# Kernel tuning notes

Measured on AMD Instinct MI355X. Metric: run time of the kernel, lower is better.

## Reference

```python
import jax, jax.numpy as jnp
import numpy as np

N_HEAD = 8
D_MODEL = 512
D_HEAD = D_MODEL // N_HEAD
D_HIDDEN = 2048
LN_EPS = 1e-5


def setup_inputs() -> dict:
    key = jax.random.key(0)
    ks = jax.random.split(key, 13)
    s = 0.02
    return {
        "spatial_features": jax.random.normal(ks[0], (4096, 64, D_MODEL), dtype=jnp.float32),
        "Wk": jax.random.normal(ks[1], (D_MODEL, D_MODEL), dtype=jnp.float32) * s,
        "bk": jnp.zeros((D_MODEL,), dtype=jnp.float32),
        "Wv": jax.random.normal(ks[2], (D_MODEL, D_MODEL), dtype=jnp.float32) * s,
        "bv": jnp.zeros((D_MODEL,), dtype=jnp.float32),
        "score_w": jax.random.normal(ks[3], (N_HEAD, D_HEAD), dtype=jnp.float32) * s,
        "score_b": jnp.zeros((N_HEAD,), dtype=jnp.float32),
        "W1": jax.random.normal(ks[4], (D_MODEL, D_HIDDEN), dtype=jnp.float32) * s,
        "b1": jnp.zeros((D_HIDDEN,), dtype=jnp.float32),
        "W2": jax.random.normal(ks[5], (D_HIDDEN, D_MODEL), dtype=jnp.float32) * s,
        "b2": jnp.zeros((D_MODEL,), dtype=jnp.float32),
        "ln_g": jnp.ones((D_MODEL,), dtype=jnp.float32),
        "ln_b": jnp.zeros((D_MODEL,), dtype=jnp.float32),
    }


def reference(spatial_features, Wk, bk, Wv, bv, score_w, score_b,
              W1, b1, W2, b2, ln_g, ln_b):
    B, N, _ = spatial_features.shape
    # k, v projections -> [B, N, H, Dh]
    k = (spatial_features @ Wk + bk).reshape(B, N, N_HEAD, D_HEAD)
    v = (spatial_features @ Wv + bv).reshape(B, N, N_HEAD, D_HEAD)
    # per-head score: Linear(d_head -> 1) batched over heads
    score = jnp.einsum('bnhd,hd->bnh', k, score_w) + score_b  # [B, N, H]
    attn = jax.nn.softmax(score, axis=1)                       # softmax over N
    # weighted sum pooling over N, then concat heads -> [B, d_model]
    feature = jnp.einsum('bnh,bnhd->bhd', attn, v).reshape(B, D_MODEL)
    # FFN with residual + layernorm (dropout = eval identity)
    h = jax.nn.gelu(feature @ W1 + b1, approximate=False)
    y = h @ W2 + b2 + feature
    mu = jnp.mean(y, axis=-1, keepdims=True)
    var = jnp.mean((y - mu) ** 2, axis=-1, keepdims=True)
    out = (y - mu) * jax.lax.rsqrt(var + LN_EPS) * ln_g + ln_b
    return out
```

## Files before the change

kernel.cpp:

```cpp
#include <hip/hip_runtime.h>
#include <hip/hip_bf16.h>

#define N_HEAD 8
#define D_MODEL 512
#define D_HEAD 64
#define D_HIDDEN 2048
#define NTOK 64
#define BATCH 4096

typedef __attribute__((ext_vector_type(4))) float f32x4;
typedef __attribute__((ext_vector_type(8))) short short8;
typedef __attribute__((ext_vector_type(8))) unsigned short u16x8;
typedef __attribute__((ext_vector_type(4))) unsigned short u16x4;

__device__ __forceinline__ float bf2f(unsigned short u) {
    return __uint_as_float(((unsigned int)u) << 16);
}
__device__ __forceinline__ unsigned short f2bf(float f) {
    unsigned int b = __float_as_uint(f);
    b += 0x7fffu + ((b >> 16) & 1u);
    return (unsigned short)(b >> 16);
}
__device__ __forceinline__ float wave_sum(float v) {
    v += __shfl_xor(v, 32); v += __shfl_xor(v, 16); v += __shfl_xor(v, 8);
    v += __shfl_xor(v, 4);  v += __shfl_xor(v, 2);  v += __shfl_xor(v, 1);
    return v;
}
__device__ __forceinline__ void gload_lds16(const void* g, void* l) {
    __builtin_amdgcn_global_load_lds(
        (const __attribute__((address_space(1))) unsigned int*)g,
        (__attribute__((address_space(3))) unsigned int*)l, 16, 0, 0);
}

__global__ __launch_bounds__(256) void prep_all(
    const float* __restrict__ Wk, const float* __restrict__ score_w,
    const float* __restrict__ Wv, const float* __restrict__ W1,
    const float* __restrict__ W2,
    unsigned short* __restrict__ uT,
    unsigned short* __restrict__ WvT, unsigned short* __restrict__ W1T,
    unsigned short* __restrict__ W2T) {
    int m = blockIdx.y;
    if (m == 3) {
        int idx = blockIdx.x * 256 + threadIdx.x;
        if (idx < 16 * 512) {
            int h = idx & 15, c = idx >> 4;
            float s = 0.f;
            if (h < 8) {
                #pragma unroll 8
                for (int d = 0; d < D_HEAD; ++d)
                    s += Wk[c * D_MODEL + h * D_HEAD + d] * score_w[h * D_HEAD + d];
            }
            uT[h * D_MODEL + c] = f2bf(s);
        }
        return;
    }
    const float* in; unsigned short* out; int K, N, tX, tiles;
    if (m == 0)      { in = Wv; out = WvT; K = 512;  N = 512;  tX = 16; tiles = 256;  }
    else if (m == 1) { in = W1; out = W1T; K = 512;  N = 2048; tX = 64; tiles = 1024; }
    else             { in = W2; out = W2T; K = 2048; N = 512;  tX = 16; tiles = 1024; }
    int t = blockIdx.x;
    if (t >= tiles) return;
    int n0 = (t % tX) * 32, k0 = (t / tX) * 32;
    __shared__ float tile[32][33];
    int tx = threadIdx.x & 31, ty = threadIdx.x >> 5;
    #pragma unroll
    for (int i = ty; i < 32; i += 8)
        tile[i][tx] = in[(size_t)(k0 + i) * N + n0 + tx];
    __syncthreads();
    #pragma unroll
    for (int i = ty; i < 32; i += 8)
        out[(size_t)(n0 + i) * K + k0 + tx] = f2bf(tile[tx][i]);
}

__global__ void score_pool_v15(
    const float* __restrict__ x, const unsigned short* __restrict__ uT,
    unsigned short* __restrict__ pooled) {
    __shared__ unsigned short xl[16 * D_MODEL];
    __shared__ unsigned short ul[8 * D_MODEL];
    __shared__ float el[16 * 8];
    __shared__ float zacc[8];

    const int tid = threadIdx.x;
    const int l = tid & 63, w = tid >> 6;
    const int hg = l >> 4, lr = l & 15;

    {
        int r = tid >> 6;
        int c8 = (tid & 63) * 8;
        u16x8 v = *(const u16x8*)(uT + r * D_MODEL + c8);
        *(u16x8*)&ul[r * D_MODEL + (c8 ^ (r << 3))] = v;
    }

    const int tr4 = tid >> 7;
    const int col4 = (tid & 127) * 4;

    const int c2 = (tid & 255) * 2;
    const int hh = tid >> 8;

    const int b0 = blockIdx.x * 4;

    float4 preA[4], preB[4];
    {
        const float4* p0 = (const float4*)(x + (size_t)b0 * (NTOK * D_MODEL));
        const float4* p1 = (const float4*)(x + (size_t)b0 * (NTOK * D_MODEL) +
                                           16 * D_MODEL);
        #pragma unroll
        for (int j = 0; j < 4; ++j) preA[j] = p0[j * 512 + tid];
        #pragma unroll
        for (int j = 0; j < 4; ++j) preB[j] = p1[j * 512 + tid];
    }

    f32x4 acc0 = {0.f, 0.f, 0.f, 0.f};
    f32x4 acc1 = {0.f, 0.f, 0.f, 0.f};

    int qq = 0;

#define QSTEP(BUF)                                                             \
    {                                                                          \
        const int q = qq & 3;                                                  \
        if (q == 0 && tid < 8) zacc[tid] = 0.f;                                \
        _Pragma("unroll")                                                      \
        for (int j = 0; j < 4; ++j) {                                          \
            int row = j * 4 + tr4;                                             \
            float4 a = BUF[j];                                                 \
            u16x4 ov = {f2bf(a.x), f2bf(a.y), f2bf(a.z), f2bf(a.w)};           \
            *(u16x4*)&xl[row * D_MODEL + (col4 ^ ((row & 7) << 3))] = ov;      \
        }                                                                      \
        if (qq < 14) {                                                         \
            const int nb = b0 + ((qq + 2) >> 2), nq = (qq + 2) & 3;            \
            const float4* p = (const float4*)(x +                              \
                (size_t)nb * (NTOK * D_MODEL) + nq * 16 * D_MODEL);            \
            _Pragma("unroll")                                                  \
            for (int j = 0; j < 4; ++j) BUF[j] = p[j * 512 + tid];             \
        }                                                                      \
        asm volatile("s_waitcnt lgkmcnt(0)" ::: "memory");                     \
        __builtin_amdgcn_s_barrier();                                   \
        if (w == (qq & 7)) {                                                   \
            f32x4 sacc = {0.f, 0.f, 0.f, 0.f};                                 \
            const int rbase = lr * D_MODEL;                                    \
            const int rsw = (lr & 7) << 3;                                     \
            _Pragma("unroll")                                                  \
            for (int ks = 0; ks < 16; ++ks) {                                  \
                int off = ks * 32 + hg * 8;                                    \
                short8 uf;                                                     \
                if (lr < 8) uf = *(const short8*)&ul[lr * D_MODEL +            \
                                                     (off ^ (lr << 3))];       \
                else        uf = (short8){0, 0, 0, 0, 0, 0, 0, 0};             \
                short8 xf = *(const short8*)&xl[rbase + (off ^ rsw)];          \
                sacc = __builtin_amdgcn_mfma_f32_16x16x32_bf16(uf, xf, sacc,   \
                                                               0, 0, 0);       \
            }                                                                  \
            f32x4 ev;                                                          \
            float zsum[4];                                                     \
            _Pragma("unroll")                                                  \
            for (int j = 0; j < 4; ++j) {                                      \
                float e = __expf(sacc[j]);                                     \
                ev[j] = e;                                                     \
                e += __shfl_xor(e, 1); e += __shfl_xor(e, 2);                  \
                e += __shfl_xor(e, 4); e += __shfl_xor(e, 8);                  \
                zsum[j] = e;                                                   \
            }                                                                  \
            if (hg < 2) {                                                      \
                *(f32x4*)&el[lr * 8 + hg * 4] = ev;                            \
                if (lr == 0) {                                                 \
                    f32x4 z = *(const f32x4*)&zacc[hg * 4];                    \
                    z[0] += zsum[0]; z[1] += zsum[1];                          \
                    z[2] += zsum[2]; z[3] += zsum[3];                          \
                    *(f32x4*)&zacc[hg * 4] = z;                                \
                }                                                              \
            }                                                                  \
        }                                                                      \
        asm volatile("s_waitcnt lgkmcnt(0)" ::: "memory");                     \
        __builtin_amdgcn_s_barrier();                                   \
        _Pragma("unroll 4")                                                    \
        for (int t = 0; t < 16; ++t) {                                         \
            unsigned int xw = *(const unsigned int*)&xl[t * D_MODEL +          \
                                                  (c2 ^ ((t & 7) << 3))];      \
            f32x4 e4 = *(const f32x4*)&el[t * 8 + hh * 4];                     \
            float xa = __uint_as_float(xw << 16);                              \
            float xb = __uint_as_float(xw & 0xffff0000u);                      \
            acc0 += e4 * xa;                                                   \
            acc1 += e4 * xb;                                                   \
        }                                                                      \
        if (q == 3) {                                                          \
            f32x4 z = *(const f32x4*)&zacc[hh * 4];                            \
            unsigned short* pb = pooled +                                      \
                (size_t)(b0 + (qq >> 2)) * (N_HEAD * D_MODEL);                 \
            _Pragma("unroll")                                                  \
            for (int hq = 0; hq < 4; ++hq) {                                   \
                float rzq = 1.f / z[hq];                                       \
                unsigned int pk = (unsigned int)f2bf(acc0[hq] * rzq) |         \
                                  ((unsigned int)f2bf(acc1[hq] * rzq) << 16);  \
                *(unsigned int*)(pb + (hh * 4 + hq) * D_MODEL + c2) = pk;      \
            }                                                                  \
            acc0 = (f32x4){0.f, 0.f, 0.f, 0.f};                                \
            acc1 = (f32x4){0.f, 0.f, 0.f, 0.f};                                \
        }                                                                      \
        asm volatile("s_waitcnt lgkmcnt(0)" ::: "memory");                     \
        __builtin_amdgcn_s_barrier();                                   \
        ++qq;                                                                  \
    }

    #pragma unroll 1
    for (int it = 0; it < 8; ++it) {
        QSTEP(preA)
        QSTEP(preB)
    }
#undef QSTEP
}

template <int BM, int BN, int MODE>
__global__ __launch_bounds__(256) void gemm_mf(
    const unsigned short* __restrict__ A, int lda,
    const unsigned short* __restrict__ BT,
    const float* __restrict__ bias,
    void* __restrict__ Cout, int ldc,
    const unsigned short* __restrict__ res, int K) {
    __shared__ unsigned short Al[BM * 64];
    __shared__ unsigned short Bl[BN * 64];
    int m0 = blockIdx.x * BM;
    int n0;
    const unsigned short* Ap = A;
    const unsigned short* Bp;
    const float* bp;
    if (MODE == 0) {
        int h = blockIdx.y;
        Ap = A + (size_t)h * 512;
        Bp = BT + (size_t)h * 64 * K;
        bp = bias + h * 64;
        n0 = h * 64;
    } else {
        n0 = blockIdx.y * BN;
        Bp = BT + (size_t)n0 * K;
        bp = bias + n0;
    }
    int tid = threadIdx.x, l = tid & 63, w = tid >> 6;
    int lr = l & 15, lq = l >> 4;
    int wm = w >> 1, wn = w & 1;
    constexpr int MR = BM / 32, NR = BN / 32;
    constexpr int AI = BM / 8, BI = BN / 8;

    f32x4 acc[MR][NR];
    #pragma unroll
    for (int mi = 0; mi < MR; ++mi)
        #pragma unroll
        for (int nj = 0; nj < NR; ++nj) acc[mi][nj] = (f32x4){0.f, 0.f, 0.f, 0.f};

    int srow = l >> 3;
    int scol = ((l & 7) ^ ((l >> 3) & 7)) << 3;

    for (int k0 = 0; k0 < K; k0 += 64) {
        #pragma unroll
        for (int j = 0; j < AI / 4; ++j) {
            int ji = w * (AI / 4) + j;
            const unsigned short* src = Ap + (size_t)(m0 + ji * 8 + srow) * lda + k0 + scol;
            gload_lds16(src, &Al[ji * 512]);
        }
        #pragma unroll
        for (int j = 0; j < BI / 4; ++j) {
            int ji = w * (BI / 4) + j;
            const unsigned short* src = Bp + (size_t)(ji * 8 + srow) * K + k0 + scol;
            gload_lds16(src, &Bl[ji * 512]);
        }
        __syncthreads();
        #pragma unroll
        for (int kk = 0; kk < 64; kk += 32) {
            int sw = (kk + lq * 8) ^ ((l & 7) << 3);
            short8 af[MR], bf[NR];
            #pragma unroll
            for (int mi = 0; mi < MR; ++mi)
                af[mi] = *(const short8*)&Al[(wm * (BM / 2) + mi * 16 + lr) * 64 + sw];
            #pragma unroll
            for (int nj = 0; nj < NR; ++nj)
                bf[nj] = *(const short8*)&Bl[(wn * (BN / 2) + nj * 16 + lr) * 64 + sw];
            #pragma unroll
            for (int mi = 0; mi < MR; ++mi)
                #pragma unroll
                for (int nj = 0; nj < NR; ++nj)
                    acc[mi][nj] = __builtin_amdgcn_mfma_f32_16x16x32_bf16(
                        af[mi], bf[nj], acc[mi][nj], 0, 0, 0);
        }
        __syncthreads();
    }

    #pragma unroll
    for (int mi = 0; mi < MR; ++mi) {
        #pragma unroll
        for (int nj = 0; nj < NR; ++nj) {
            #pragma unroll
            for (int j = 0; j < 4; ++j) {
                int row = m0 + wm * (BM / 2) + mi * 16 + lq * 4 + j;
                int nl = wn * (BN / 2) + nj * 16 + lr;
                int col = n0 + nl;
                float v = acc[mi][nj][j] + bp[nl];
                if (MODE == 1) {
                    v = 0.5f * v * (1.0f + erff(v * 0.70710678118654752f));
                }
                if (MODE == 2) {
                    v += bf2f(res[(size_t)row * 512 + col]);
                    ((float*)Cout)[(size_t)row * ldc + col] = v;
                } else {
                    ((unsigned short*)Cout)[(size_t)row * ldc + col] = f2bf(v);
                }
            }
        }
    }
}

__global__ __launch_bounds__(256) void ln_kernel(
    float* __restrict__ y, const float* __restrict__ g, const float* __restrict__ bta) {
    int row = blockIdx.x * 4 + (threadIdx.x >> 6);
    int l = threadIdx.x & 63;
    float* yp = y + (size_t)row * D_MODEL;
    float4 v0 = *(const float4*)(yp + l * 8);
    float4 v1 = *(const float4*)(yp + l * 8 + 4);
    float vv[8] = {v0.x, v0.y, v0.z, v0.w, v1.x, v1.y, v1.z, v1.w};
    float s = 0.f;
    #pragma unroll
    for (int i = 0; i < 8; ++i) s += vv[i];
    s = wave_sum(s);
    float mean = s * (1.f / 512.f);
    float q = 0.f;
    #pragma unroll
    for (int i = 0; i < 8; ++i) { float d = vv[i] - mean; q += d * d; }
    q = wave_sum(q);
    float rstd = rsqrtf(q * (1.f / 512.f) + 1e-5f);
    float4 g0 = *(const float4*)(g + l * 8);
    float4 g1 = *(const float4*)(g + l * 8 + 4);
    float4 b0 = *(const float4*)(bta + l * 8);
    float4 b1 = *(const float4*)(bta + l * 8 + 4);
    float gv[8] = {g0.x, g0.y, g0.z, g0.w, g1.x, g1.y, g1.z, g1.w};
    float bv[8] = {b0.x, b0.y, b0.z, b0.w, b1.x, b1.y, b1.z, b1.w};
    float ov[8];
    #pragma unroll
    for (int i = 0; i < 8; ++i) ov[i] = (vv[i] - mean) * rstd * gv[i] + bv[i];
    float4 o0 = {ov[0], ov[1], ov[2], ov[3]};
    float4 o1 = {ov[4], ov[5], ov[6], ov[7]};
    *(float4*)(yp + l * 8) = o0;
    *(float4*)(yp + l * 8 + 4) = o1;
}

extern "C" void kernel_launch(void* const* d_in, const int* in_sizes, int n_in,
                              void* d_out, int out_size, void* d_ws, size_t ws_size,
                              hipStream_t stream) {
    const float* x       = (const float*)d_in[0];
    const float* Wk      = (const float*)d_in[1];
    const float* Wv      = (const float*)d_in[3];
    const float* bv      = (const float*)d_in[4];
    const float* score_w = (const float*)d_in[5];
    const float* W1      = (const float*)d_in[7];
    const float* b1      = (const float*)d_in[8];
    const float* W2      = (const float*)d_in[9];
    const float* b2      = (const float*)d_in[10];
    const float* ln_g    = (const float*)d_in[11];
    const float* ln_b    = (const float*)d_in[12];
    float* out = (float*)d_out;

    char* ws = (char*)d_ws;
    size_t off = 0;
    auto alloc = [&](size_t sz) {
        void* p = ws + off;
        off = (off + sz + 1023) & ~(size_t)1023;
        return p;
    };
    unsigned short* uT  = (unsigned short*)alloc((size_t)16 * D_MODEL * 2);
    unsigned short* WvT = (unsigned short*)alloc((size_t)512 * 512 * 2);
    unsigned short* W1T = (unsigned short*)alloc((size_t)2048 * 512 * 2);
    unsigned short* W2T = (unsigned short*)alloc((size_t)512 * 2048 * 2);
    unsigned short* pooled = (unsigned short*)alloc((size_t)BATCH * N_HEAD * D_MODEL * 2);
    unsigned short* feat   = (unsigned short*)alloc((size_t)BATCH * D_MODEL * 2);
    unsigned short* Hbuf   = (unsigned short*)alloc((size_t)BATCH * D_HIDDEN * 2);

    prep_all<<<dim3(1024, 4), dim3(256), 0, stream>>>(
        Wk, score_w, Wv, W1, W2, uT, WvT, W1T, W2T);
    score_pool_v15<<<dim3(1024), dim3(512), 0, stream>>>(x, uT, pooled);
    gemm_mf<128, 64, 0><<<dim3(32, 8), dim3(256), 0, stream>>>(
        pooled, N_HEAD * D_MODEL, WvT, bv, (void*)feat, D_MODEL,
        (const unsigned short*)nullptr, 512);
    gemm_mf<128, 128, 1><<<dim3(32, 16), dim3(256), 0, stream>>>(
        feat, D_MODEL, W1T, b1, (void*)Hbuf, D_HIDDEN,
        (const unsigned short*)nullptr, 512);
    gemm_mf<64, 128, 2><<<dim3(64, 4), dim3(256), 0, stream>>>(
        Hbuf, D_HIDDEN, W2T, b2, (void*)out, D_MODEL, feat, 2048);
    ln_kernel<<<dim3(1024), dim3(256), 0, stream>>>(out, ln_g, ln_b);
}
```

Measured before the change: 209.9 us.

## Software-pipeline score/pool kernel across three LDS stages with one barrier per step

Restructures the score+pool loop into a three-stage pipeline. Each step stores tile qq to LDS, computes scores for tile qq-1 and does the weighted pooling for tile qq-2, using a triple-buffered x tile and double-buffered exp/normaliser arrays. This cuts the barriers per step from two to one and lets the single-wave MFMA score work overlap with the pooling FMAs. It costs more LDS (three 16KB x buffers) and adds two extra drain iterations, which may lower occupancy.

```diff
diff --git a/kernel.cpp b/kernel.cpp
--- a/kernel.cpp
+++ b/kernel.cpp
@@ -72,13 +72,13 @@
         out[(size_t)(n0 + i) * K + k0 + tx] = f2bf(tile[tx][i]);
 }
 
-__global__ void score_pool_v15(
+__global__ __launch_bounds__(512) void score_pool_v16(
     const float* __restrict__ x, const unsigned short* __restrict__ uT,
     unsigned short* __restrict__ pooled) {
-    __shared__ unsigned short xl[16 * D_MODEL];
+    __shared__ unsigned short xl[3][16 * D_MODEL];
     __shared__ unsigned short ul[8 * D_MODEL];
-    __shared__ float el[16 * 8];
-    __shared__ float zacc[8];
+    __shared__ float el[2][16 * 8];
+    __shared__ float zacc[2][8];
 
     const int tid = threadIdx.x;
     const int l = tid & 63, w = tid >> 6;
@@ -117,25 +117,29 @@
 
 #define QSTEP(BUF)                                                             \
     {                                                                          \
-        const int q = qq & 3;                                                  \
-        if (q == 0 && tid < 8) zacc[tid] = 0.f;                                \
-        _Pragma("unroll")                                                      \
-        for (int j = 0; j < 4; ++j) {                                          \
-            int row = j * 4 + tr4;                                             \
-            float4 a = BUF[j];                                                 \
-            u16x4 ov = {f2bf(a.x), f2bf(a.y), f2bf(a.z), f2bf(a.w)};           \
-            *(u16x4*)&xl[row * D_MODEL + (col4 ^ ((row & 7) << 3))] = ov;      \
+        const int s_i  = qq % 3;                                               \
+        const int sc_i = (qq + 2) % 3;                       \
+        const int p_i  = (qq + 1) % 3;                       \
+        if (qq < 16) {                                                         \
+            _Pragma("unroll")                                                  \
+            for (int j = 0; j < 4; ++j) {                                      \
+                int row = j * 4 + tr4;                                         \
+                float4 a = BUF[j];                                             \
+                u16x4 ov = {f2bf(a.x), f2bf(a.y), f2bf(a.z), f2bf(a.w)};       \
+                *(u16x4*)&xl[s_i][row * D_MODEL +                              \
+                              (col4 ^ ((row & 7) << 3))] = ov;                 \
+            }                                                                  \
+            if (qq < 14) {                                                     \
+                const int nt = qq + 2;                                         \
+                const int nb = b0 + (nt >> 2), nq = nt & 3;                    \
+                const float4* p = (const float4*)(x +                          \
+                    (size_t)nb * (NTOK * D_MODEL) + nq * 16 * D_MODEL);        \
+                _Pragma("unroll")                                              \
+                for (int j = 0; j < 4; ++j) BUF[j] = p[j * 512 + tid];         \
+            }                                                                  \
         }                                                                      \
-        if (qq < 14) {                                                         \
-            const int nb = b0 + ((qq + 2) >> 2), nq = (qq + 2) & 3;            \
-            const float4* p = (const float4*)(x +                              \
-                (size_t)nb * (NTOK * D_MODEL) + nq * 16 * D_MODEL);            \
-            _Pragma("unroll")                                                  \
-            for (int j = 0; j < 4; ++j) BUF[j] = p[j * 512 + tid];             \
-        }                                                                      \
-        asm volatile("s_waitcnt lgkmcnt(0)" ::: "memory");                     \
-        __builtin_amdgcn_s_barrier();                                   \
-        if (w == (qq & 7)) {                                                   \
+        if (qq >= 1 && qq <= 16 && w == ((qq - 1) & 7)) {                      \
+            const int t = qq - 1;                                              \
             f32x4 sacc = {0.f, 0.f, 0.f, 0.f};                                 \
             const int rbase = lr * D_MODEL;                                    \
             const int rsw = (lr & 7) << 3;                                     \
@@ -146,7 +150,7 @@
                 if (lr < 8) uf = *(const short8*)&ul[lr * D_MODEL +            \
                                                      (off ^ (lr << 3))];       \
                 else        uf = (short8){0, 0, 0, 0, 0, 0, 0, 0};             \
-                short8 xf = *(const short8*)&xl[rbase + (off ^ rsw)];          \
+                short8 xf = *(const short8*)&xl[sc_i][rbase + (off ^ rsw)];    \
                 sacc = __builtin_amdgcn_mfma_f32_16x16x32_bf16(uf, xf, sacc,   \
                                                                0, 0, 0);       \
             }                                                                  \
@@ -161,48 +165,55 @@
                 zsum[j] = e;                                                   \
             }                                                                  \
             if (hg < 2) {                                                      \
-                *(f32x4*)&el[lr * 8 + hg * 4] = ev;                            \
+                *(f32x4*)&el[t & 1][lr * 8 + hg * 4] = ev;                     \
                 if (lr == 0) {                                                 \
-                    f32x4 z = *(const f32x4*)&zacc[hg * 4];                    \
-                    z[0] += zsum[0]; z[1] += zsum[1];                          \
-                    z[2] += zsum[2]; z[3] += zsum[3];                          \
-                    *(f32x4*)&zacc[hg * 4] = z;                                \
+                    const int zb = (t >> 2) & 1;                               \
+                    f32x4 z;                                                   \
+                    if ((t & 3) == 0) {                                        \
+                        z = (f32x4){zsum[0], zsum[1], zsum[2], zsum[3]};       \
+                    } else {                                                   \
+                        z = *(const f32x4*)&zacc[zb][hg * 4];                  \
+                        z[0] += zsum[0]; z[1] += zsum[1];                      \
+                        z[2] += zsum[2]; z[3] += zsum[3];                      \
+                    }                                                          \
+                    *(f32x4*)&zacc[zb][hg * 4] = z;                            \
                 }                                                              \
+            }                                                                  \
+        }                                                                      \
+        if (qq >= 2) {                                                         \
+            const int t = qq - 2;                                              \
+            _Pragma("unroll 4")                                                \
+            for (int tk = 0; tk < 16; ++tk) {                                  \
+                unsigned int xw = *(const unsigned int*)&xl[p_i][tk * D_MODEL +\
+                                                    (c2 ^ ((tk & 7) << 3))];   \
+                f32x4 e4 = *(const f32x4*)&el[t & 1][tk * 8 + hh * 4];         \
+                float xa = __uint_as_float(xw << 16);                          \
+                float xb = __uint_as_float(xw & 0xffff0000u);                  \
+                acc0 += e4 * xa;                                               \
+                acc1 += e4 * xb;                                               \
+            }                                                                  \
+            if ((t & 3) == 3) {                                                \
+                f32x4 z = *(const f32x4*)&zacc[(t >> 2) & 1][hh * 4];          \
+                unsigned short* pb = pooled +                                  \
+                    (size_t)(b0 + (t >> 2)) * (N_HEAD * D_MODEL);              \
+                _Pragma("unroll")                                              \
+                for (int hq = 0; hq < 4; ++hq) {                               \
+                    float rzq = 1.f / z[hq];                                   \
+                    unsigned int pk = (unsigned int)f2bf(acc0[hq] * rzq) |     \
+                                  ((unsigned int)f2bf(acc1[hq] * rzq) << 16);  \
+                    *(unsigned int*)(pb + (hh * 4 + hq) * D_MODEL + c2) = pk;  \
+                }                                                              \
+                acc0 = (f32x4){0.f, 0.f, 0.f, 0.f};                            \
+                acc1 = (f32x4){0.f, 0.f, 0.f, 0.f};                            \
             }                                                                  \
         }                                                                      \
         asm volatile("s_waitcnt lgkmcnt(0)" ::: "memory");                     \
-        __builtin_amdgcn_s_barrier();                                   \
-        _Pragma("unroll 4")                                                    \
-        for (int t = 0; t < 16; ++t) {                                         \
-            unsigned int xw = *(const unsigned int*)&xl[t * D_MODEL +          \
-                                                  (c2 ^ ((t & 7) << 3))];      \
-            f32x4 e4 = *(const f32x4*)&el[t * 8 + hh * 4];                     \
-            float xa = __uint_as_float(xw << 16);                              \
-            float xb = __uint_as_float(xw & 0xffff0000u);                      \
-            acc0 += e4 * xa;                                                   \
-            acc1 += e4 * xb;                                                   \
-        }                                                                      \
-        if (q == 3) {                                                          \
-            f32x4 z = *(const f32x4*)&zacc[hh * 4];                            \
-            unsigned short* pb = pooled +                                      \
-                (size_t)(b0 + (qq >> 2)) * (N_HEAD * D_MODEL);                 \
-            _Pragma("unroll")                                                  \
-            for (int hq = 0; hq < 4; ++hq) {                                   \
-                float rzq = 1.f / z[hq];                                       \
-                unsigned int pk = (unsigned int)f2bf(acc0[hq] * rzq) |         \
-                                  ((unsigned int)f2bf(acc1[hq] * rzq) << 16);  \
-                *(unsigned int*)(pb + (hh * 4 + hq) * D_MODEL + c2) = pk;      \
-            }                                                                  \
-            acc0 = (f32x4){0.f, 0.f, 0.f, 0.f};                                \
-            acc1 = (f32x4){0.f, 0.f, 0.f, 0.f};                                \
-        }                                                                      \
-        asm volatile("s_waitcnt lgkmcnt(0)" ::: "memory");                     \
-        __builtin_amdgcn_s_barrier();                                   \
+        __builtin_amdgcn_s_barrier();                                          \
         ++qq;                                                                  \
     }
 
     #pragma unroll 1
-    for (int it = 0; it < 8; ++it) {
+    for (int it = 0; it < 9; ++it) {
         QSTEP(preA)
         QSTEP(preB)
     }
@@ -373,7 +384,7 @@
 
     prep_all<<<dim3(1024, 4), dim3(256), 0, stream>>>(
         Wk, score_w, Wv, W1, W2, uT, WvT, W1T, W2T);
-    score_pool_v15<<<dim3(1024), dim3(512), 0, stream>>>(x, uT, pooled);
+    score_pool_v16<<<dim3(1024), dim3(512), 0, stream>>>(x, uT, pooled);
     gemm_mf<128, 64, 0><<<dim3(32, 8), dim3(256), 0, stream>>>(
         pooled, N_HEAD * D_MODEL, WvT, bv, (void*)feat, D_MODEL,
         (const unsigned short*)nullptr, 512);
```

Result: no change. 210.8 us (+0.4%).

## Pool from fp32 registers instead of rereading bf16 tile from LDS

Applied to the files above, without the earlier changes.

Changes the thread-to-data mapping of the score/pool kernel so each thread keeps its loaded fp32 x values and accumulates the attention-weighted sum for 4 columns across all 8 heads directly from registers. Cross-token partial sums are reduced with wave shuffles at the end of each batch element. It also delays issuing the next prefetch until after pooling. This removes the per-token LDS reads of the bf16 x tile and pools at fp32 precision. In exchange it uses more accumulator registers and adds shuffle reductions, and the prefetch now has less time to hide its latency.

```diff
diff --git a/kernel.cpp b/kernel.cpp
--- a/kernel.cpp
+++ b/kernel.cpp
@@ -72,7 +72,7 @@
         out[(size_t)(n0 + i) * K + k0 + tx] = f2bf(tile[tx][i]);
 }
 
-__global__ void score_pool_v15(
+__global__ void score_pool_v18(
     const float* __restrict__ x, const unsigned short* __restrict__ uT,
     unsigned short* __restrict__ pooled) {
     __shared__ unsigned short xl[16 * D_MODEL];
@@ -91,47 +91,41 @@
         *(u16x8*)&ul[r * D_MODEL + (c8 ^ (r << 3))] = v;
     }
 
-    const int tr4 = tid >> 7;
-    const int col4 = (tid & 127) * 4;
-
-    const int c2 = (tid & 255) * 2;
-    const int hh = tid >> 8;
+    const int tg = l >> 4;
+    const int cq = w * 16 + (l & 15);
+    const int col4 = cq * 4;
 
     const int b0 = blockIdx.x * 4;
 
     float4 preA[4], preB[4];
     {
         const float4* p0 = (const float4*)(x + (size_t)b0 * (NTOK * D_MODEL));
-        const float4* p1 = (const float4*)(x + (size_t)b0 * (NTOK * D_MODEL) +
-                                           16 * D_MODEL);
-        #pragma unroll
-        for (int j = 0; j < 4; ++j) preA[j] = p0[j * 512 + tid];
-        #pragma unroll
-        for (int j = 0; j < 4; ++j) preB[j] = p1[j * 512 + tid];
-    }
-
-    f32x4 acc0 = {0.f, 0.f, 0.f, 0.f};
-    f32x4 acc1 = {0.f, 0.f, 0.f, 0.f};
+        const float4* p1 = p0 + 16 * 128;
+        #pragma unroll
+        for (int j = 0; j < 4; ++j) preA[j] = p0[(4 * j + tg) * 128 + cq];
+        #pragma unroll
+        for (int j = 0; j < 4; ++j) preB[j] = p1[(4 * j + tg) * 128 + cq];
+    }
+
+    f32x4 acc[4][2];
+    #pragma unroll
+    for (int c = 0; c < 4; ++c) {
+        acc[c][0] = (f32x4){0.f, 0.f, 0.f, 0.f};
+        acc[c][1] = (f32x4){0.f, 0.f, 0.f, 0.f};
+    }
 
     int qq = 0;
 
-#define QSTEP(BUF)                                                             \
+#define QSTEP(CUR)                                                             \
     {                                                                          \
         const int q = qq & 3;                                                  \
         if (q == 0 && tid < 8) zacc[tid] = 0.f;                                \
         _Pragma("unroll")                                                      \
         for (int j = 0; j < 4; ++j) {                                          \
-            int row = j * 4 + tr4;                                             \
-            float4 a = BUF[j];                                                 \
+            int row = 4 * j + tg;                                              \
+            float4 a = CUR[j];                                                 \
             u16x4 ov = {f2bf(a.x), f2bf(a.y), f2bf(a.z), f2bf(a.w)};           \
             *(u16x4*)&xl[row * D_MODEL + (col4 ^ ((row & 7) << 3))] = ov;      \
-        }                                                                      \
-        if (qq < 14) {                                                         \
-            const int nb = b0 + ((qq + 2) >> 2), nq = (qq + 2) & 3;            \
-            const float4* p = (const float4*)(x +                              \
-                (size_t)nb * (NTOK * D_MODEL) + nq * 16 * D_MODEL);            \
-            _Pragma("unroll")                                                  \
-            for (int j = 0; j < 4; ++j) BUF[j] = p[j * 512 + tid];             \
         }                                                                      \
         asm volatile("s_waitcnt lgkmcnt(0)" ::: "memory");                     \
         __builtin_amdgcn_s_barrier();                                   \
@@ -172,29 +166,61 @@
         }                                                                      \
         asm volatile("s_waitcnt lgkmcnt(0)" ::: "memory");                     \
         __builtin_amdgcn_s_barrier();                                   \
-        _Pragma("unroll 4")                                                    \
-        for (int t = 0; t < 16; ++t) {                                         \
-            unsigned int xw = *(const unsigned int*)&xl[t * D_MODEL +          \
-                                                  (c2 ^ ((t & 7) << 3))];      \
-            f32x4 e4 = *(const f32x4*)&el[t * 8 + hh * 4];                     \
-            float xa = __uint_as_float(xw << 16);                              \
-            float xb = __uint_as_float(xw & 0xffff0000u);                      \
-            acc0 += e4 * xa;                                                   \
-            acc1 += e4 * xb;                                                   \
+        _Pragma("unroll")                                                      \
+        for (int j = 0; j < 4; ++j) {                                          \
+            int t = 4 * j + tg;                                                \
+            f32x4 e0 = *(const f32x4*)&el[t * 8];                              \
+            f32x4 e1 = *(const f32x4*)&el[t * 8 + 4];                          \
+            float4 a = CUR[j];                                                 \
+            acc[0][0] += e0 * a.x; acc[0][1] += e1 * a.x;                      \
+            acc[1][0] += e0 * a.y; acc[1][1] += e1 * a.y;                      \
+            acc[2][0] += e0 * a.z; acc[2][1] += e1 * a.z;                      \
+            acc[3][0] += e0 * a.w; acc[3][1] += e1 * a.w;                      \
+        }                                                                      \
+        if (qq < 14) {                                                         \
+            const int nt = qq + 2;                                             \
+            const float4* p = (const float4*)(x +                              \
+                (size_t)(b0 + (nt >> 2)) * (NTOK * D_MODEL) +                  \
+                (nt & 3) * 16 * D_MODEL);                                      \
+            _Pragma("unroll")                                                  \
+            for (int j = 0; j < 4; ++j) CUR[j] = p[(4 * j + tg) * 128 + cq];   \
         }                                                                      \
         if (q == 3) {                                                          \
-            f32x4 z = *(const f32x4*)&zacc[hh * 4];                            \
-            unsigned short* pb = pooled +                                      \
-                (size_t)(b0 + (qq >> 2)) * (N_HEAD * D_MODEL);                 \
+              \
             _Pragma("unroll")                                                  \
-            for (int hq = 0; hq < 4; ++hq) {                                   \
-                float rzq = 1.f / z[hq];                                       \
-                unsigned int pk = (unsigned int)f2bf(acc0[hq] * rzq) |         \
-                                  ((unsigned int)f2bf(acc1[hq] * rzq) << 16);  \
-                *(unsigned int*)(pb + (hh * 4 + hq) * D_MODEL + c2) = pk;      \
-            }                                                                  \
-            acc0 = (f32x4){0.f, 0.f, 0.f, 0.f};                                \
-            acc1 = (f32x4){0.f, 0.f, 0.f, 0.f};                                \
+            for (int c = 0; c < 4; ++c) {                                      \
+                _Pragma("unroll")                                              \
+                for (int hhh = 0; hhh < 2; ++hhh) {                            \
+                    _Pragma("unroll")                                          \
+                    for (int k = 0; k < 4; ++k) {                              \
+                        float v = acc[c][hhh][k];                              \
+                        v += __shfl_xor(v, 16);                                \
+                        v += __shfl_xor(v, 32);                                \
+                        acc[c][hhh][k] = v;                                    \
+                    }                                                          \
+                }                                                              \
+            }                                                                  \
+            if (l < 16) {                                                      \
+                f32x4 z0 = *(const f32x4*)&zacc[0];                            \
+                f32x4 z1 = *(const f32x4*)&zacc[4];                            \
+                unsigned short* pb = pooled +                                  \
+                    (size_t)(b0 + (qq >> 2)) * (N_HEAD * D_MODEL);             \
+                _Pragma("unroll")                                              \
+                for (int h = 0; h < 8; ++h) {                                  \
+                    const int hhh = h >> 2, hi = h & 3;                        \
+                    float rzh = 1.f / (h < 4 ? z0[hi] : z1[hi]);               \
+                    u16x4 o = {f2bf(acc[0][hhh][hi] * rzh),                    \
+                               f2bf(acc[1][hhh][hi] * rzh),                    \
+                               f2bf(acc[2][hhh][hi] * rzh),                    \
+                               f2bf(acc[3][hhh][hi] * rzh)};                   \
+                    *(u16x4*)&pb[h * D_MODEL + col4] = o;                      \
+                }                                                              \
+            }                                                                  \
+            _Pragma("unroll")                                                  \
+            for (int c = 0; c < 4; ++c) {                                      \
+                acc[c][0] = (f32x4){0.f, 0.f, 0.f, 0.f};                       \
+                acc[c][1] = (f32x4){0.f, 0.f, 0.f, 0.f};                       \
+            }                                                                  \
         }                                                                      \
         asm volatile("s_waitcnt lgkmcnt(0)" ::: "memory");                     \
         __builtin_amdgcn_s_barrier();                                   \
@@ -373,7 +399,7 @@
 
     prep_all<<<dim3(1024, 4), dim3(256), 0, stream>>>(
         Wk, score_w, Wv, W1, W2, uT, WvT, W1T, W2T);
-    score_pool_v15<<<dim3(1024), dim3(512), 0, stream>>>(x, uT, pooled);
+    score_pool_v18<<<dim3(1024), dim3(512), 0, stream>>>(x, uT, pooled);
     gemm_mf<128, 64, 0><<<dim3(32, 8), dim3(256), 0, stream>>>(
         pooled, N_HEAD * D_MODEL, WvT, bv, (void*)feat, D_MODEL,
         (const unsigned short*)nullptr, 512);
```

Measured after the change: 759.8 us. 262% more time.
